# Optimization experiments

Hardware: AMD Instinct MI355X
Metric: run time of the kernel (lower is better)

## Reference

```python
import jax, jax.numpy as jnp
import numpy as np

N_NODES, N_EDGES = 50000, 800000
IN_DIM, OUT_DIM, EDGE_DIM = 128, 128, 32
NUM_HEADS = 8
HEAD_DIM = OUT_DIM // NUM_HEADS
SCALE = HEAD_DIM ** -0.5


def setup_inputs() -> dict:
    key = jax.random.key(0)
    ks = jax.random.split(key, 8)
    def lin_w(k, fan_in, fan_out):
        # kaiming-uniform-ish init like nn.Linear
        bound = 1.0 / np.sqrt(fan_in)
        return jax.random.uniform(k, (fan_in, fan_out), jnp.float32, -bound, bound)
    return {
        "node_features": jax.random.normal(ks[0], (N_NODES, IN_DIM), jnp.float32),
        "edge_features": jax.random.normal(ks[1], (N_EDGES, EDGE_DIM), jnp.float32),
        "Wq": lin_w(ks[2], IN_DIM, OUT_DIM), "bq": jnp.zeros((OUT_DIM,), jnp.float32),
        "Wk": lin_w(ks[3], IN_DIM, OUT_DIM), "bk": jnp.zeros((OUT_DIM,), jnp.float32),
        "Wv": lin_w(ks[4], IN_DIM, OUT_DIM), "bv": jnp.zeros((OUT_DIM,), jnp.float32),
        "We": lin_w(ks[5], EDGE_DIM, OUT_DIM), "be": jnp.zeros((OUT_DIM,), jnp.float32),
        "edge_list": jax.random.randint(ks[6], (N_EDGES, 2), 0, N_NODES, jnp.int32),
        "num_nodes": N_NODES,
    }


def reference(node_features, edge_features, Wq, bq, Wk, bk, Wv, bv, We, be, edge_list, num_nodes):
    # node projections -> [N, H, D]
    Q = (node_features @ Wq + bq).reshape(-1, NUM_HEADS, HEAD_DIM)
    K = (node_features @ Wk + bk).reshape(-1, NUM_HEADS, HEAD_DIM)
    V = (node_features @ Wv + bv).reshape(-1, NUM_HEADS, HEAD_DIM)
    edge_bias = (edge_features @ We + be).reshape(-1, NUM_HEADS, HEAD_DIM)

    src = edge_list[:, 0]  # node_in
    dst = edge_list[:, 1]  # node_out

    # per-edge per-head scores: [E, H]
    scores = jnp.einsum("ehd,ehd->eh", Q[src], K[dst]) * SCALE + edge_bias.sum(-1)
    # NOTE: softmax over the HEADS axis (dim=1), exactly as in the source
    weights = jax.nn.softmax(scores, axis=1)

    # weighted messages gathered from src, scattered to dst: [E, H, D] -> [N, H, D]
    msg = V[src] * weights[..., None]
    node_updates = jax.ops.segment_sum(msg, dst, num_segments=num_nodes)
    return node_updates.reshape(num_nodes, OUT_DIM)
```

## Files before the change

### kernel.cpp

```cpp
#include <hip/hip_runtime.h>
#include <math.h>

#define IN_DIM   128
#define OUT_DIM  128
#define EDGE_DIM 32
#define NUM_HEADS 8
#define HEAD_DIM 16
#define SCALE 0.25f

typedef __attribute__((ext_vector_type(8))) short bf16x8;
typedef __attribute__((ext_vector_type(4))) float f32x4;
typedef __attribute__((ext_vector_type(4))) unsigned int u32x4;

__device__ inline unsigned short f2bf(float x) {
    unsigned int u = __float_as_uint(x);
    unsigned int r = u + 0x7fff + ((u >> 16) & 1);
    return (unsigned short)(r >> 16);
}
__device__ inline float bflo(unsigned int u) { return __uint_as_float(u << 16); }
__device__ inline float bfhi(unsigned int u) { return __uint_as_float(u & 0xffff0000u); }

__global__ __launch_bounds__(256) void setup_kernel(
    int* __restrict__ counts, int n_nodes, int nbz,
    const float* __restrict__ Wq, const float* __restrict__ Wk,
    const float* __restrict__ Wv, unsigned short* __restrict__ WtB, int nbw,
    const float* __restrict__ We, const float* __restrict__ be,
    float* __restrict__ WeR, float* __restrict__ beR)
{
    const int bx = blockIdx.x;
    const int t  = threadIdx.x;
    if (bx < nbz) {
        const int i = bx * 256 + t;
        if (i < n_nodes) counts[i] = 0;
    } else if (bx < nbz + nbw) {
        const int idx = (bx - nbz) * 256 + t;
        const int mat = idx >> 14;
        const int rem = idx & 16383;
        const int n = rem >> 7, k = rem & 127;
        const float* W = (mat == 0) ? Wq : (mat == 1) ? Wk : Wv;
        WtB[mat * 16384 + n * 128 + k] = f2bf(W[k * 128 + n]);
    } else {
        const int k = t >> 3, h = t & 7;
        float s = 0.f;
#pragma unroll
        for (int d = 0; d < HEAD_DIM; ++d) s += We[k * OUT_DIM + h * HEAD_DIM + d];
        WeR[k * NUM_HEADS + h] = s;
        if (t < NUM_HEADS) {
            float sb = 0.f;
#pragma unroll
            for (int d = 0; d < HEAD_DIM; ++d) sb += be[t * HEAD_DIM + d];
            beR[t] = sb;
        }
    }
}

__global__ __launch_bounds__(256) void mega_kernel(
    const int* __restrict__ el, int* __restrict__ counts, int* __restrict__ rank,
    const float* __restrict__ ef, const float* __restrict__ WeR,
    const float* __restrict__ beR, unsigned int* __restrict__ ebias_e,
    int n_edges, int nbh,
    const float* __restrict__ X, const unsigned short* __restrict__ WtB,
    const float* __restrict__ bq, const float* __restrict__ bk,
    const float* __restrict__ bv,
    unsigned short* __restrict__ QVb, unsigned short* __restrict__ Kb,
    int n_nodes, int nbq)
{
    const int bx = blockIdx.x;
    const int t  = threadIdx.x;

    if (bx < nbh) {
        __shared__ float WeRs[EDGE_DIM * NUM_HEADS];
        __shared__ float beRs[NUM_HEADS];
        WeRs[t] = WeR[t];
        if (t < NUM_HEADS) beRs[t] = beR[t];
        __syncthreads();

        const int e = bx * 256 + t;
        if (e >= n_edges) return;
        const int2 ed = ((const int2*)el)[e];
        rank[e] = atomicAdd(&counts[ed.y], 1);

        float acc[NUM_HEADS];
#pragma unroll
        for (int h = 0; h < NUM_HEADS; ++h) acc[h] = beRs[h];
        const f32x4* efr = (const f32x4*)(ef + (size_t)e * EDGE_DIM);
#pragma unroll
        for (int kk = 0; kk < 8; ++kk) {
            const f32x4 f = efr[kk];
            const float* w0 = &WeRs[(kk * 4 + 0) * NUM_HEADS];
            const float* w1 = &WeRs[(kk * 4 + 1) * NUM_HEADS];
            const float* w2 = &WeRs[(kk * 4 + 2) * NUM_HEADS];
            const float* w3 = &WeRs[(kk * 4 + 3) * NUM_HEADS];
#pragma unroll
            for (int h = 0; h < NUM_HEADS; ++h)
                acc[h] = fmaf(f[0], w0[h], fmaf(f[1], w1[h], fmaf(f[2], w2[h], fmaf(f[3], w3[h], acc[h]))));
        }
        u32x4 pk;
        pk[0] = (unsigned)f2bf(acc[0]) | ((unsigned)f2bf(acc[1]) << 16);
        pk[1] = (unsigned)f2bf(acc[2]) | ((unsigned)f2bf(acc[3]) << 16);
        pk[2] = (unsigned)f2bf(acc[4]) | ((unsigned)f2bf(acc[5]) << 16);
        pk[3] = (unsigned)f2bf(acc[6]) | ((unsigned)f2bf(acc[7]) << 16);
        *(u32x4*)(ebias_e + (size_t)e * 4) = pk;
    } else {
        __shared__ unsigned short stg[4][16][136];

        const int idx   = bx - nbh;
        const int which = idx / nbq;
        const int mb    = idx - which * nbq;
        const float* bias = (which == 0) ? bq : (which == 1) ? bk : bv;
        const unsigned short* Wg = WtB + which * 16384;

        const int wave = t >> 6, lane = t & 63;
        const int quad = lane >> 4, li = lane & 15;
        const int m0 = mb * 64 + wave * 16;
        int mrow = m0 + li;
        if (mrow >= n_nodes) mrow = n_nodes - 1;

        f32x4 acc[8];
#pragma unroll
        for (int nt = 0; nt < 8; ++nt) acc[nt] = (f32x4){0.f, 0.f, 0.f, 0.f};

#pragma unroll
        for (int ks = 0; ks < 4; ++ks) {
            const f32x4* xr = (const f32x4*)(X + (size_t)mrow * 128 + ks * 32 + quad * 8);
            const f32x4 x0 = xr[0], x1 = xr[1];
            bf16x8 a;
            a[0] = (short)f2bf(x0[0]); a[1] = (short)f2bf(x0[1]);
            a[2] = (short)f2bf(x0[2]); a[3] = (short)f2bf(x0[3]);
            a[4] = (short)f2bf(x1[0]); a[5] = (short)f2bf(x1[1]);
            a[6] = (short)f2bf(x1[2]); a[7] = (short)f2bf(x1[3]);
#pragma unroll
            for (int nt = 0; nt < 8; ++nt) {
                const bf16x8 b = *(const bf16x8*)(Wg + (nt * 16 + li) * 128 + ks * 32 + quad * 8);
                acc[nt] = __builtin_amdgcn_mfma_f32_16x16x32_bf16(a, b, acc[nt], 0, 0, 0);
            }
        }

#pragma unroll
        for (int nt = 0; nt < 8; ++nt) {
            const float bb = bias[nt * 16 + li];
#pragma unroll
            for (int r = 0; r < 4; ++r)
                stg[wave][quad * 4 + r][nt * 16 + li] = f2bf(acc[nt][r] + bb);
        }
        __syncthreads();

        const int R = lane >> 2;
        const int c = lane & 3;
        const int node = m0 + R;
        if (node < n_nodes) {
            const u32x4* s = (const u32x4*)(&stg[wave][R][c * 32]);
            u32x4 d0 = s[0], d1 = s[1], d2 = s[2], d3 = s[3];
            unsigned short* dp =
                (which == 0) ? (QVb + (size_t)node * 256 + c * 32)
              : (which == 1) ? (Kb  + (size_t)node * 128 + c * 32)
              :                (QVb + (size_t)node * 256 + 128 + c * 32);
            u32x4* d = (u32x4*)dp;
            d[0] = d0; d[1] = d1; d[2] = d2; d[3] = d3;
        }
    }
}

__global__ __launch_bounds__(256) void scan1_kernel(
    const int* __restrict__ counts, int* __restrict__ bsums, int n)
{
    __shared__ int lds[256];
    const int i = blockIdx.x * 256 + threadIdx.x;
    lds[threadIdx.x] = (i < n) ? counts[i] : 0;
    __syncthreads();
    for (int off = 128; off > 0; off >>= 1) {
        if (threadIdx.x < off) lds[threadIdx.x] += lds[threadIdx.x + off];
        __syncthreads();
    }
    if (threadIdx.x == 0) bsums[blockIdx.x] = lds[0];
}

__global__ __launch_bounds__(256) void scan3_kernel(
    const int* __restrict__ counts, const int* __restrict__ bsums,
    int* __restrict__ offsets, int n, int n_edges, int nb)
{
    __shared__ int lds[256];
    const int t = threadIdx.x;

    int v = (t < nb) ? bsums[t] : 0;
    lds[t] = v;
    __syncthreads();
    for (int off = 1; off < 256; off <<= 1) {
        const int u = (t >= off) ? lds[t - off] : 0;
        __syncthreads();
        lds[t] += u;
        __syncthreads();
    }
    const int base = (blockIdx.x > 0) ? lds[blockIdx.x - 1] : 0;
    __syncthreads();

    const int i = blockIdx.x * 256 + t;
    const int c = (i < n) ? counts[i] : 0;
    lds[t] = c;
    __syncthreads();
    for (int off = 1; off < 256; off <<= 1) {
        const int u = (t >= off) ? lds[t - off] : 0;
        __syncthreads();
        lds[t] += u;
        __syncthreads();
    }
    if (i < n) offsets[i] = base + lds[t] - c;
    if (blockIdx.x == 0 && t == 0) offsets[n] = n_edges;
}

__global__ __launch_bounds__(256) void scatter_kernel(
    const int* __restrict__ el, const int* __restrict__ rank,
    const unsigned int* __restrict__ ebias_e,
    const int* __restrict__ offsets, unsigned int* __restrict__ recs,
    int n_edges)
{
    const int e = blockIdx.x * 256 + threadIdx.x;
    if (e >= n_edges) return;
    const int2 ed = ((const int2*)el)[e];
    const u32x4 eb = *(const u32x4*)(ebias_e + (size_t)e * 4);
    const int pos = offsets[ed.y] + rank[e];

    u32x4 r0, r1;
    r0[0] = (unsigned)ed.x;
    r0[1] = 0;
    r0[2] = eb[0];
    r0[3] = eb[1];
    r1[0] = eb[2];
    r1[1] = eb[3];
    r1[2] = 0; r1[3] = 0;
    u32x4* rp = (u32x4*)(recs + (size_t)pos * 8);
    rp[0] = r0;
    rp[1] = r1;
}

__global__ __launch_bounds__(256) void aggregate_kernel(
    const unsigned short* __restrict__ QVb, const unsigned short* __restrict__ Kb,
    const int* __restrict__ offsets, const unsigned int* __restrict__ recs,
    float* __restrict__ out, int n_nodes)
{
    const int gw   = (blockIdx.x * 256 + threadIdx.x) >> 6;
    const int lane = threadIdx.x & 63;
    const int half = lane >> 5, ln = lane & 31;
    const int node = gw * 2 + half;
    const int h = ln >> 2;
    const bool valid = node < n_nodes;

    int beg = 0, end = 0;
    if (valid) { beg = offsets[node]; end = offsets[node + 1]; }
    const int cnt = end - beg;
    const int mcnt = max(cnt, __shfl_xor(cnt, 32));

    float k0 = 0.f, k1 = 0.f, k2 = 0.f, k3 = 0.f;
    if (valid) {
        const uint2 kp = ((const uint2*)(Kb + (size_t)node * 128))[ln];
        k0 = bflo(kp.x); k1 = bfhi(kp.x); k2 = bflo(kp.y); k3 = bfhi(kp.y);
    }

    float a0 = 0.f, a1 = 0.f, a2 = 0.f, a3 = 0.f;

    uint2 qp = make_uint2(0, 0), vp = make_uint2(0, 0);
    float eb = 0.f;
    if (cnt > 0) {
        const unsigned int* rb = recs + (size_t)beg * 8;
        const int src = (int)rb[0];
        const unsigned int ebp = rb[2 + (h >> 1)];
        eb = (h & 1) ? bfhi(ebp) : bflo(ebp);
        const uint2* r = (const uint2*)(QVb + (size_t)src * 256);
        qp = r[ln];
        vp = r[32 + ln];
    }

    for (int i = 0; i < mcnt; ++i) {
        uint2 nqp = qp, nvp = vp;
        float neb = eb;
        if (i + 1 < cnt) {
            const unsigned int* rb = recs + (size_t)(beg + i + 1) * 8;
            const int ns = (int)rb[0];
            const unsigned int ebp = rb[2 + (h >> 1)];
            neb = (h & 1) ? bfhi(ebp) : bflo(ebp);
            const uint2* r = (const uint2*)(QVb + (size_t)ns * 256);
            nqp = r[ln];
            nvp = r[32 + ln];
        }

        const float q0 = bflo(qp.x), q1 = bfhi(qp.x);
        const float q2 = bflo(qp.y), q3 = bfhi(qp.y);
        float p = fmaf(q0, k0, fmaf(q1, k1, fmaf(q2, k2, q3 * k3)));
        p += __shfl_xor(p, 1);
        p += __shfl_xor(p, 2);
        const float score = fmaf(p, SCALE, eb);

        float mx = score;
        mx = fmaxf(mx, __shfl_xor(mx, 4));
        mx = fmaxf(mx, __shfl_xor(mx, 8));
        mx = fmaxf(mx, __shfl_xor(mx, 16));
        const float ex = __expf(score - mx);
        float den = ex;
        den += __shfl_xor(den, 4);
        den += __shfl_xor(den, 8);
        den += __shfl_xor(den, 16);
        const float w = __fdividef(ex, den);

        if (i < cnt) {
            a0 = fmaf(w, bflo(vp.x), a0);
            a1 = fmaf(w, bfhi(vp.x), a1);
            a2 = fmaf(w, bflo(vp.y), a2);
            a3 = fmaf(w, bfhi(vp.y), a3);
        }
        qp = nqp; vp = nvp; eb = neb;
    }

    if (valid) {
        f32x4 o; o[0] = a0; o[1] = a1; o[2] = a2; o[3] = a3;
        *(((f32x4*)(out + (size_t)node * OUT_DIM)) + ln) = o;
    }
}

extern "C" void kernel_launch(void* const* d_in, const int* in_sizes, int n_in,
                              void* d_out, int out_size, void* d_ws, size_t ws_size,
                              hipStream_t stream)
{
    const float* X   = (const float*)d_in[0];
    const float* ef  = (const float*)d_in[1];
    const float* Wq  = (const float*)d_in[2];
    const float* bq  = (const float*)d_in[3];
    const float* Wk  = (const float*)d_in[4];
    const float* bk  = (const float*)d_in[5];
    const float* Wv  = (const float*)d_in[6];
    const float* bv  = (const float*)d_in[7];
    const float* We  = (const float*)d_in[8];
    const float* be  = (const float*)d_in[9];
    const int*   el  = (const int*)d_in[10];

    const int n_nodes = in_sizes[0] / IN_DIM;
    const int n_edges = in_sizes[10] / 2;

    char* w = (char*)d_ws;
    auto alloc = [&](size_t bytes) { char* p = w; w += (bytes + 255) & ~(size_t)255; return p; };

    unsigned short* QVb    = (unsigned short*)alloc((size_t)n_nodes * 256 * 2);
    unsigned short* Kb     = (unsigned short*)alloc((size_t)n_nodes * 128 * 2);
    unsigned short* WtB    = (unsigned short*)alloc((size_t)3 * 128 * 128 * 2);
    unsigned int*   recs   = (unsigned int*)alloc((size_t)n_edges * 32);
    unsigned int*   ebias_e= (unsigned int*)alloc((size_t)n_edges * 16);
    int* rank    = (int*)alloc((size_t)n_edges * 4);
    float* WeR   = (float*)alloc(EDGE_DIM * NUM_HEADS * 4);
    float* beR   = (float*)alloc(NUM_HEADS * 4);
    int* counts  = (int*)alloc((size_t)n_nodes * 4);
    int* offsets = (int*)alloc((size_t)(n_nodes + 1) * 4);
    int* bsums   = (int*)alloc(256 * 4);

    const int nbz = (n_nodes + 255) / 256;
    const int nbw = (3 * 128 * 128) / 256;
    setup_kernel<<<nbz + nbw + 1, 256, 0, stream>>>(
        counts, n_nodes, nbz, Wq, Wk, Wv, WtB, nbw, We, be, WeR, beR);

    const int nbh = (n_edges + 255) / 256;
    const int nbq = (n_nodes + 63) / 64;
    mega_kernel<<<nbh + 3 * nbq, 256, 0, stream>>>(
        el, counts, rank, ef, WeR, beR, ebias_e, n_edges, nbh,
        X, WtB, bq, bk, bv, QVb, Kb, n_nodes, nbq);

    const int nb = (n_nodes + 255) / 256;
    scan1_kernel<<<nb, 256, 0, stream>>>(counts, bsums, n_nodes);
    scan3_kernel<<<nb, 256, 0, stream>>>(counts, bsums, offsets, n_nodes, n_edges, nb);

    scatter_kernel<<<(n_edges + 255) / 256, 256, 0, stream>>>(
        el, rank, ebias_e, offsets, recs, n_edges);

    const int nwaves = (n_nodes + 1) / 2;
    aggregate_kernel<<<(nwaves * 64 + 255) / 256, 256, 0, stream>>>(
        QVb, Kb, offsets, recs, (float*)d_out, n_nodes);
}
```

Before: 349.3 us.

## Move edge-bias projection into scatter, pre-convert X to bf16, fuse QKV blocks

The per-edge edge-bias projection moves out of the mega kernel into the scatter kernel, which removes the intermediate ebias_e buffer (a write and a re-read of 16 bytes per edge). The setup kernel now converts X to bf16 once. Each mega-kernel block then loads its X tile a single time and computes all three Q/K/V projections in a loop, instead of three separate blocks each reading and converting fp32 X. The cost is an extra Xb buffer written and read, added per-thread work in the scatter kernel, and WeR read from global memory there rather than from LDS.

```diff
diff --git a/kernel.cpp b/kernel.cpp
--- a/kernel.cpp
+++ b/kernel.cpp
@@ -25,7 +25,8 @@
     const float* __restrict__ Wq, const float* __restrict__ Wk,
     const float* __restrict__ Wv, unsigned short* __restrict__ WtB, int nbw,
     const float* __restrict__ We, const float* __restrict__ be,
-    float* __restrict__ WeR, float* __restrict__ beR)
+    float* __restrict__ WeR, float* __restrict__ beR,
+    const float* __restrict__ X, unsigned short* __restrict__ Xb)
 {
     const int bx = blockIdx.x;
     const int t  = threadIdx.x;
@@ -39,7 +40,7 @@
         const int n = rem >> 7, k = rem & 127;
         const float* W = (mat == 0) ? Wq : (mat == 1) ? Wk : Wv;
         WtB[mat * 16384 + n * 128 + k] = f2bf(W[k * 128 + n]);
-    } else {
+    } else if (bx == nbz + nbw) {
         const int k = t >> 3, h = t & 7;
         float s = 0.f;
 #pragma unroll
@@ -51,88 +52,74 @@
             for (int d = 0; d < HEAD_DIM; ++d) sb += be[t * HEAD_DIM + d];
             beR[t] = sb;
         }
+    } else {
+        const int i = (bx - (nbz + nbw + 1)) * 256 + t;
+        if (i < n_nodes * 16) {
+            const f32x4* xr = (const f32x4*)(X + (size_t)i * 8);
+            const f32x4 x0 = xr[0], x1 = xr[1];
+            u32x4 p;
+            p[0] = (unsigned)f2bf(x0[0]) | ((unsigned)f2bf(x0[1]) << 16);
+            p[1] = (unsigned)f2bf(x0[2]) | ((unsigned)f2bf(x0[3]) << 16);
+            p[2] = (unsigned)f2bf(x1[0]) | ((unsigned)f2bf(x1[1]) << 16);
+            p[3] = (unsigned)f2bf(x1[2]) | ((unsigned)f2bf(x1[3]) << 16);
+            *(u32x4*)(Xb + (size_t)i * 8) = p;
+        }
     }
 }
 
 __global__ __launch_bounds__(256) void mega_kernel(
-    const int* __restrict__ el, int* __restrict__ counts, int* __restrict__ rank,
-    const float* __restrict__ ef, const float* __restrict__ WeR,
-    const float* __restrict__ beR, unsigned int* __restrict__ ebias_e,
-    int n_edges, int nbh,
-    const float* __restrict__ X, const unsigned short* __restrict__ WtB,
+    const unsigned short* __restrict__ Xb, const unsigned short* __restrict__ WtB,
     const float* __restrict__ bq, const float* __restrict__ bk,
     const float* __restrict__ bv,
     unsigned short* __restrict__ QVb, unsigned short* __restrict__ Kb,
-    int n_nodes, int nbq)
+    int n_nodes, int nbq,
+    const int* __restrict__ el, int* __restrict__ counts,
+    int* __restrict__ rank, int n_edges)
 {
     const int bx = blockIdx.x;
     const int t  = threadIdx.x;
 
-    if (bx < nbh) {
-        __shared__ float WeRs[EDGE_DIM * NUM_HEADS];
-        __shared__ float beRs[NUM_HEADS];
-        WeRs[t] = WeR[t];
-        if (t < NUM_HEADS) beRs[t] = beR[t];
-        __syncthreads();
-
-        const int e = bx * 256 + t;
-        if (e >= n_edges) return;
-        const int2 ed = ((const int2*)el)[e];
-        rank[e] = atomicAdd(&counts[ed.y], 1);
-
-        float acc[NUM_HEADS];
-#pragma unroll
-        for (int h = 0; h < NUM_HEADS; ++h) acc[h] = beRs[h];
-        const f32x4* efr = (const f32x4*)(ef + (size_t)e * EDGE_DIM);
-#pragma unroll
-        for (int kk = 0; kk < 8; ++kk) {
-            const f32x4 f = efr[kk];
-            const float* w0 = &WeRs[(kk * 4 + 0) * NUM_HEADS];
-            const float* w1 = &WeRs[(kk * 4 + 1) * NUM_HEADS];
-            const float* w2 = &WeRs[(kk * 4 + 2) * NUM_HEADS];
-            const float* w3 = &WeRs[(kk * 4 + 3) * NUM_HEADS];
-#pragma unroll
-            for (int h = 0; h < NUM_HEADS; ++h)
-                acc[h] = fmaf(f[0], w0[h], fmaf(f[1], w1[h], fmaf(f[2], w2[h], fmaf(f[3], w3[h], acc[h]))));
-        }
-        u32x4 pk;
-        pk[0] = (unsigned)f2bf(acc[0]) | ((unsigned)f2bf(acc[1]) << 16);
-        pk[1] = (unsigned)f2bf(acc[2]) | ((unsigned)f2bf(acc[3]) << 16);
-        pk[2] = (unsigned)f2bf(acc[4]) | ((unsigned)f2bf(acc[5]) << 16);
-        pk[3] = (unsigned)f2bf(acc[6]) | ((unsigned)f2bf(acc[7]) << 16);
-        *(u32x4*)(ebias_e + (size_t)e * 4) = pk;
-    } else {
-        __shared__ unsigned short stg[4][16][136];
-
-        const int idx   = bx - nbh;
-        const int which = idx / nbq;
-        const int mb    = idx - which * nbq;
+    if (bx >= nbq) {
+        const int e = (bx - nbq) * 256 + t;
+        if (e < n_edges) {
+            const int2 ed = ((const int2*)el)[e];
+            rank[e] = atomicAdd(&counts[ed.y], 1);
+        }
+        return;
+    }
+
+    __shared__ unsigned short stg[4][16][136];
+
+    const int wave = t >> 6, lane = t & 63;
+    const int quad = lane >> 4, li = lane & 15;
+    const int m0 = bx * 64 + wave * 16;
+    int mrow = m0 + li;
+    if (mrow >= n_nodes) mrow = n_nodes - 1;
+
+    bf16x8 a[4];
+#pragma unroll
+    for (int ks = 0; ks < 4; ++ks)
+        a[ks] = *(const bf16x8*)(Xb + (size_t)mrow * 128 + ks * 32 + quad * 8);
+
+    const int R = lane >> 2;
+    const int cc = lane & 3;
+    const int node = m0 + R;
+
+#pragma unroll
+    for (int which = 0; which < 3; ++which) {
         const float* bias = (which == 0) ? bq : (which == 1) ? bk : bv;
         const unsigned short* Wg = WtB + which * 16384;
 
-        const int wave = t >> 6, lane = t & 63;
-        const int quad = lane >> 4, li = lane & 15;
-        const int m0 = mb * 64 + wave * 16;
-        int mrow = m0 + li;
-        if (mrow >= n_nodes) mrow = n_nodes - 1;
-
         f32x4 acc[8];
 #pragma unroll
         for (int nt = 0; nt < 8; ++nt) acc[nt] = (f32x4){0.f, 0.f, 0.f, 0.f};
 
 #pragma unroll
         for (int ks = 0; ks < 4; ++ks) {
-            const f32x4* xr = (const f32x4*)(X + (size_t)mrow * 128 + ks * 32 + quad * 8);
-            const f32x4 x0 = xr[0], x1 = xr[1];
-            bf16x8 a;
-            a[0] = (short)f2bf(x0[0]); a[1] = (short)f2bf(x0[1]);
-            a[2] = (short)f2bf(x0[2]); a[3] = (short)f2bf(x0[3]);
-            a[4] = (short)f2bf(x1[0]); a[5] = (short)f2bf(x1[1]);
-            a[6] = (short)f2bf(x1[2]); a[7] = (short)f2bf(x1[3]);
 #pragma unroll
             for (int nt = 0; nt < 8; ++nt) {
                 const bf16x8 b = *(const bf16x8*)(Wg + (nt * 16 + li) * 128 + ks * 32 + quad * 8);
-                acc[nt] = __builtin_amdgcn_mfma_f32_16x16x32_bf16(a, b, acc[nt], 0, 0, 0);
+                acc[nt] = __builtin_amdgcn_mfma_f32_16x16x32_bf16(a[ks], b, acc[nt], 0, 0, 0);
             }
         }
 
@@ -145,19 +132,17 @@
         }
         __syncthreads();
 
-        const int R = lane >> 2;
-        const int c = lane & 3;
-        const int node = m0 + R;
         if (node < n_nodes) {
-            const u32x4* s = (const u32x4*)(&stg[wave][R][c * 32]);
+            const u32x4* s = (const u32x4*)(&stg[wave][R][cc * 32]);
             u32x4 d0 = s[0], d1 = s[1], d2 = s[2], d3 = s[3];
             unsigned short* dp =
-                (which == 0) ? (QVb + (size_t)node * 256 + c * 32)
-              : (which == 1) ? (Kb  + (size_t)node * 128 + c * 32)
-              :                (QVb + (size_t)node * 256 + 128 + c * 32);
+                (which == 0) ? (QVb + (size_t)node * 256 + cc * 32)
+              : (which == 1) ? (Kb  + (size_t)node * 128 + cc * 32)
+              :                (QVb + (size_t)node * 256 + 128 + cc * 32);
             u32x4* d = (u32x4*)dp;
             d[0] = d0; d[1] = d1; d[2] = d2; d[3] = d3;
         }
+        __syncthreads();
     }
 }
 
@@ -210,23 +195,40 @@
 
 __global__ __launch_bounds__(256) void scatter_kernel(
     const int* __restrict__ el, const int* __restrict__ rank,
-    const unsigned int* __restrict__ ebias_e,
+    const float* __restrict__ ef,
+    const float* __restrict__ WeR, const float* __restrict__ beR,
     const int* __restrict__ offsets, unsigned int* __restrict__ recs,
     int n_edges)
 {
     const int e = blockIdx.x * 256 + threadIdx.x;
     if (e >= n_edges) return;
     const int2 ed = ((const int2*)el)[e];
-    const u32x4 eb = *(const u32x4*)(ebias_e + (size_t)e * 4);
     const int pos = offsets[ed.y] + rank[e];
+
+    float acc[NUM_HEADS];
+#pragma unroll
+    for (int h = 0; h < NUM_HEADS; ++h) acc[h] = beR[h];
+
+    const f32x4* efr = (const f32x4*)(ef + (size_t)e * EDGE_DIM);
+#pragma unroll
+    for (int kk = 0; kk < 8; ++kk) {
+        const f32x4 f = efr[kk];
+#pragma unroll
+        for (int c = 0; c < 4; ++c) {
+            const float* wr = WeR + (kk * 4 + c) * NUM_HEADS;
+#pragma unroll
+            for (int h = 0; h < NUM_HEADS; ++h)
+                acc[h] = fmaf(f[c], wr[h], acc[h]);
+        }
+    }
 
     u32x4 r0, r1;
     r0[0] = (unsigned)ed.x;
     r0[1] = 0;
-    r0[2] = eb[0];
-    r0[3] = eb[1];
-    r1[0] = eb[2];
-    r1[1] = eb[3];
+    r0[2] = (unsigned)f2bf(acc[0]) | ((unsigned)f2bf(acc[1]) << 16);
+    r0[3] = (unsigned)f2bf(acc[2]) | ((unsigned)f2bf(acc[3]) << 16);
+    r1[0] = (unsigned)f2bf(acc[4]) | ((unsigned)f2bf(acc[5]) << 16);
+    r1[1] = (unsigned)f2bf(acc[6]) | ((unsigned)f2bf(acc[7]) << 16);
     r1[2] = 0; r1[3] = 0;
     u32x4* rp = (u32x4*)(recs + (size_t)pos * 8);
     rp[0] = r0;
@@ -341,8 +343,8 @@
     unsigned short* QVb    = (unsigned short*)alloc((size_t)n_nodes * 256 * 2);
     unsigned short* Kb     = (unsigned short*)alloc((size_t)n_nodes * 128 * 2);
     unsigned short* WtB    = (unsigned short*)alloc((size_t)3 * 128 * 128 * 2);
+    unsigned short* Xb     = (unsigned short*)alloc((size_t)n_nodes * 128 * 2);
     unsigned int*   recs   = (unsigned int*)alloc((size_t)n_edges * 32);
-    unsigned int*   ebias_e= (unsigned int*)alloc((size_t)n_edges * 16);
     int* rank    = (int*)alloc((size_t)n_edges * 4);
     float* WeR   = (float*)alloc(EDGE_DIM * NUM_HEADS * 4);
     float* beR   = (float*)alloc(NUM_HEADS * 4);
@@ -352,21 +354,22 @@
 
     const int nbz = (n_nodes + 255) / 256;
     const int nbw = (3 * 128 * 128) / 256;
-    setup_kernel<<<nbz + nbw + 1, 256, 0, stream>>>(
-        counts, n_nodes, nbz, Wq, Wk, Wv, WtB, nbw, We, be, WeR, beR);
+    const int nbx = (n_nodes * 16 + 255) / 256;
+    setup_kernel<<<nbz + nbw + 1 + nbx, 256, 0, stream>>>(
+        counts, n_nodes, nbz, Wq, Wk, Wv, WtB, nbw, We, be, WeR, beR, X, Xb);
 
     const int nbh = (n_edges + 255) / 256;
     const int nbq = (n_nodes + 63) / 64;
-    mega_kernel<<<nbh + 3 * nbq, 256, 0, stream>>>(
-        el, counts, rank, ef, WeR, beR, ebias_e, n_edges, nbh,
-        X, WtB, bq, bk, bv, QVb, Kb, n_nodes, nbq);
+    mega_kernel<<<nbq + nbh, 256, 0, stream>>>(
+        Xb, WtB, bq, bk, bv, QVb, Kb, n_nodes, nbq,
+        el, counts, rank, n_edges);
 
     const int nb = (n_nodes + 255) / 256;
     scan1_kernel<<<nb, 256, 0, stream>>>(counts, bsums, n_nodes);
     scan3_kernel<<<nb, 256, 0, stream>>>(counts, bsums, offsets, n_nodes, n_edges, nb);
 
-    scatter_kernel<<<(n_edges + 255) / 256, 256, 0, stream>>>(
-        el, rank, ebias_e, offsets, recs, n_edges);
+    scatter_kernel<<<nbh, 256, 0, stream>>>(
+        el, rank, ef, WeR, beR, offsets, recs, n_edges);
 
     const int nwaves = (n_nodes + 1) / 2;
     aggregate_kernel<<<(nwaves * 64 + 255) / 256, 256, 0, stream>>>(
```

New measurement: 384.3 us. 1.1x slower.
